# Optimization experiments

Measured on AMD Instinct MI355X. Metric: run time of the kernel, lower is better.

The kernel has to match this reference:

```python
import jax, jax.numpy as jnp
import numpy as np

B = 4096
D = 128
TEMP = 0.5
EPS = 1e-8  # torch cosine_similarity norm clamp


def setup_inputs() -> dict:
    key = jax.random.key(0)
    k1, k2 = jax.random.split(key)
    zi = jax.random.normal(k1, (B, D), dtype=jnp.float32)
    zj = jax.random.normal(k2, (B, D), dtype=jnp.float32)
    return {"zi": zi, "zj": zj}


def reference(zi, zj):
    b = zi.shape[0]
    n2 = 2 * b
    z = jnp.concatenate([zi, zj], axis=0)                      # (2N, D)
    norm = jnp.maximum(jnp.linalg.norm(z, axis=-1, keepdims=True), EPS)
    zn = z / norm
    sim = zn @ zn.T                                            # (2N, 2N) cosine similarity
    # positives: torch.diag(sim, +B) and torch.diag(sim, -B)
    right = jnp.diagonal(sim, offset=b)                        # sim[i, i+B]
    left = jnp.diagonal(sim, offset=-b)                        # sim[i+B, i]
    pos = jnp.concatenate([left, right]) / TEMP                # (2N,)
    # logits row i = [pos_i] + all sims except self-diagonal and the positive,
    # so the softmax denominator set = all entries except the self-diagonal.
    logits = sim / TEMP
    neg_big = jnp.asarray(jnp.finfo(logits.dtype).min, logits.dtype)
    masked = jnp.where(jnp.eye(n2, dtype=bool), neg_big, logits)
    lse = jax.nn.logsumexp(masked, axis=1)                     # (2N,)
    # CrossEntropyLoss(reduction='sum') with label 0, then / 2N
    loss = jnp.sum(lse - pos) / n2
    return loss
```

## Files before the change

### kernel.cpp

```cpp
#include <hip/hip_runtime.h>
#include <hip/hip_bf16.h>


#define BB 4096
#define N2 8192
#define DD 128
#define CSPLIT 16
#define CW (N2 / CSPLIT)
#define NCT (CW / 16)

using bf16 = __hip_bfloat16;
typedef __attribute__((ext_vector_type(8))) short short8;
typedef __attribute__((ext_vector_type(4))) float float4v;

__global__ __launch_bounds__(256) void ntx_norm_kernel(
    const float* __restrict__ zi, const float* __restrict__ zj,
    bf16* __restrict__ zn, float* __restrict__ rowsum, float* __restrict__ pos) {
  const int wave = threadIdx.x >> 6;
  const int lane = threadIdx.x & 63;
  const int row = blockIdx.x * 4 + wave;
  const float* own = (row < BB) ? (zi + (size_t)row * DD)
                                : (zj + (size_t)(row - BB) * DD);
  const float* par = (row < BB) ? (zj + (size_t)row * DD)
                                : (zi + (size_t)(row - BB) * DD);
  float2 v = ((const float2*)own)[lane];
  float2 w = ((const float2*)par)[lane];
  float s1 = v.x * v.x + v.y * v.y;
  float s2 = w.x * w.x + w.y * w.y;
  float s3 = v.x * w.x + v.y * w.y;
  #pragma unroll
  for (int o = 32; o > 0; o >>= 1) {
    s1 += __shfl_xor(s1, o);
    s2 += __shfl_xor(s2, o);
    s3 += __shfl_xor(s3, o);
  }
  float nv = fmaxf(sqrtf(s1), 1e-8f);
  float nw = fmaxf(sqrtf(s2), 1e-8f);
  float rv = 1.0f / nv;
  bf16 bx = __float2bfloat16(v.x * rv);
  bf16 by = __float2bfloat16(v.y * rv);
  __hip_bfloat162 h2; h2.x = bx; h2.y = by;
  ((__hip_bfloat162*)(zn + (size_t)row * DD))[lane] = h2;
  float fx = __bfloat162float(bx), fy = __bfloat162float(by);
  float sii = fx * fx + fy * fy;
  #pragma unroll
  for (int o = 32; o > 0; o >>= 1) sii += __shfl_xor(sii, o);
  if (lane == 0) {
    rowsum[row] = -__expf(2.0f * sii);
    pos[row] = s3 / (nv * nw);
  }
}

__global__ __launch_bounds__(256) void ntx_sim_kernel(
    const bf16* __restrict__ zn, float* __restrict__ rowsum) {
  const int wave = threadIdx.x >> 6;
  const int lane = threadIdx.x & 63;
  const int quad = lane >> 4;
  const int l15  = lane & 15;
  const short* zs = (const short*)zn;

  const int rowBase = blockIdx.y * 256 + wave * 64;
  const int colBase0 = blockIdx.x * CW;

  short8 a[4][4];
  #pragma unroll
  for (int t = 0; t < 4; t++) {
    const short* ap = zs + (size_t)(rowBase + t * 16 + l15) * DD + quad * 8;
    #pragma unroll
    for (int c = 0; c < 4; c++) a[t][c] = *(const short8*)(ap + c * 32);
  }

  float rs[4][4];
  #pragma unroll
  for (int t = 0; t < 4; t++)
    #pragma unroll
    for (int r = 0; r < 4; r++) rs[t][r] = 0.0f;

  const short* bbase = zs + (size_t)(colBase0 + l15) * DD + quad * 8;

  short8 b[4];
  #pragma unroll
  for (int c = 0; c < 4; c++) b[c] = *(const short8*)(bbase + c * 32);

  for (int ct = 0; ct < NCT; ct++) {
    const int nct = (ct + 1) & (NCT - 1);
    const short* bp = bbase + (size_t)nct * 16 * DD;
    short8 bn[4];
    #pragma unroll
    for (int c = 0; c < 4; c++) bn[c] = *(const short8*)(bp + c * 32);

    #pragma unroll
    for (int t = 0; t < 4; t++) {
      float4v acc = {0.f, 0.f, 0.f, 0.f};
      acc = __builtin_amdgcn_mfma_f32_16x16x32_bf16(a[t][0], b[0], acc, 0, 0, 0);
      acc = __builtin_amdgcn_mfma_f32_16x16x32_bf16(a[t][1], b[1], acc, 0, 0, 0);
      acc = __builtin_amdgcn_mfma_f32_16x16x32_bf16(a[t][2], b[2], acc, 0, 0, 0);
      acc = __builtin_amdgcn_mfma_f32_16x16x32_bf16(a[t][3], b[3], acc, 0, 0, 0);
      #pragma unroll
      for (int r = 0; r < 4; r++) rs[t][r] += __expf(acc[r] * 2.0f);
    }

    #pragma unroll
    for (int c = 0; c < 4; c++) b[c] = bn[c];
  }

  #pragma unroll
  for (int t = 0; t < 4; t++) {
    #pragma unroll
    for (int r = 0; r < 4; r++) {
      float s = rs[t][r];
      s += __shfl_xor(s, 1);
      s += __shfl_xor(s, 2);
      s += __shfl_xor(s, 4);
      s += __shfl_xor(s, 8);
      if (l15 == 0)
        atomicAdd(&rowsum[rowBase + t * 16 + quad * 4 + r], s);
    }
  }
}

__global__ __launch_bounds__(1024) void ntx_finalize_kernel(
    const float* __restrict__ rowsum, const float* __restrict__ pos,
    float* __restrict__ out) {
  float s = 0.f;
  for (int i = threadIdx.x; i < N2; i += 1024)
    s += __logf(rowsum[i]) - 2.0f * pos[i];
  #pragma unroll
  for (int o = 32; o > 0; o >>= 1) s += __shfl_xor(s, o);
  __shared__ float sm[16];
  const int wave = threadIdx.x >> 6;
  const int lane = threadIdx.x & 63;
  if (lane == 0) sm[wave] = s;
  __syncthreads();
  if (threadIdx.x == 0) {
    float t = 0.f;
    #pragma unroll
    for (int i = 0; i < 16; i++) t += sm[i];
    out[0] = t / (float)N2;
  }
}

extern "C" void kernel_launch(void* const* d_in, const int* in_sizes, int n_in,
                              void* d_out, int out_size, void* d_ws, size_t ws_size,
                              hipStream_t stream) {
  const float* zi = (const float*)d_in[0];
  const float* zj = (const float*)d_in[1];
  float* out = (float*)d_out;

  char* ws = (char*)d_ws;
  bf16* zn = (bf16*)ws;
  float* rowsum = (float*)(ws + (size_t)N2 * DD * 2);
  float* pos = rowsum + N2;

  ntx_norm_kernel<<<N2 / 4, 256, 0, stream>>>(zi, zj, zn, rowsum, pos);
  dim3 grid(CSPLIT, N2 / 256);
  ntx_sim_kernel<<<grid, 256, 0, stream>>>(zn, rowsum);
  ntx_finalize_kernel<<<1, 1024, 0, stream>>>(rowsum, pos, out);
}
```

Baseline: 100.6 us.

## Stage B tiles in LDS via async DMA, prescale by log2e, fuse finalize

```diff
diff --git a/kernel.cpp b/kernel.cpp
--- a/kernel.cpp
+++ b/kernel.cpp
@@ -1,24 +1,38 @@
 #include <hip/hip_runtime.h>
 #include <hip/hip_bf16.h>
+#include <stdint.h>
 
 
 #define BB 4096
 #define N2 8192
 #define DD 128
-#define CSPLIT 16
+#define CSPLIT 32
 #define CW (N2 / CSPLIT)
-#define NCT (CW / 16)
+#define STAGE 64
+#define NCHUNK (CW / STAGE)
+#define NBLOCKS (CSPLIT * (N2 / 256))
+#define TWO_LOG2E 2.8853900817779268f
 
 using bf16 = __hip_bfloat16;
 typedef __attribute__((ext_vector_type(8))) short short8;
 typedef __attribute__((ext_vector_type(4))) float float4v;
 
+__device__ inline void load_lds16(const void* g, void* l) {
+  __builtin_amdgcn_global_load_lds(
+      (const __attribute__((address_space(1))) uint32_t*)g,
+      (__attribute__((address_space(3))) uint32_t*)(uint32_t)(uintptr_t)l,
+      16, 0, 0);
+}
+
 __global__ __launch_bounds__(256) void ntx_norm_kernel(
     const float* __restrict__ zi, const float* __restrict__ zj,
-    bf16* __restrict__ zn, float* __restrict__ rowsum, float* __restrict__ pos) {
+    bf16* __restrict__ zn, bf16* __restrict__ zn_s,
+    float* __restrict__ rowsum, float* __restrict__ pos,
+    int* __restrict__ counter) {
   const int wave = threadIdx.x >> 6;
   const int lane = threadIdx.x & 63;
   const int row = blockIdx.x * 4 + wave;
+  if (blockIdx.x == 0 && threadIdx.x == 0) counter[0] = 0;
   const float* own = (row < BB) ? (zi + (size_t)row * DD)
                                 : (zj + (size_t)(row - BB) * DD);
   const float* par = (row < BB) ? (zj + (size_t)row * DD)
@@ -39,33 +53,44 @@
   float rv = 1.0f / nv;
   bf16 bx = __float2bfloat16(v.x * rv);
   bf16 by = __float2bfloat16(v.y * rv);
+  bf16 sx = __float2bfloat16(v.x * rv * TWO_LOG2E);
+  bf16 sy = __float2bfloat16(v.y * rv * TWO_LOG2E);
   __hip_bfloat162 h2; h2.x = bx; h2.y = by;
   ((__hip_bfloat162*)(zn + (size_t)row * DD))[lane] = h2;
-  float fx = __bfloat162float(bx), fy = __bfloat162float(by);
-  float sii = fx * fx + fy * fy;
+  __hip_bfloat162 g2; g2.x = sx; g2.y = sy;
+  ((__hip_bfloat162*)(zn_s + (size_t)row * DD))[lane] = g2;
+  float sii = __bfloat162float(sx) * __bfloat162float(bx) +
+              __bfloat162float(sy) * __bfloat162float(by);
   #pragma unroll
   for (int o = 32; o > 0; o >>= 1) sii += __shfl_xor(sii, o);
   if (lane == 0) {
-    rowsum[row] = -__expf(2.0f * sii);
+    rowsum[row] = -__builtin_amdgcn_exp2f(sii);
     pos[row] = s3 / (nv * nw);
   }
 }
 
 __global__ __launch_bounds__(256) void ntx_sim_kernel(
-    const bf16* __restrict__ zn, float* __restrict__ rowsum) {
-  const int wave = threadIdx.x >> 6;
-  const int lane = threadIdx.x & 63;
+    const bf16* __restrict__ zn, const bf16* __restrict__ zn_s,
+    float* __restrict__ rowsum, const float* __restrict__ pos,
+    int* __restrict__ counter, float* __restrict__ out) {
+  __shared__ short lds[2][STAGE * DD];
+  __shared__ int lastFlag;
+  __shared__ float sm[4];
+  const int tid  = threadIdx.x;
+  const int wave = tid >> 6;
+  const int lane = tid & 63;
   const int quad = lane >> 4;
   const int l15  = lane & 15;
-  const short* zs = (const short*)zn;
-
-  const int rowBase = blockIdx.y * 256 + wave * 64;
+  const short* zs  = (const short*)zn;
+  const short* zss = (const short*)zn_s;
+
+  const int rowBase  = blockIdx.y * 256 + wave * 64;
   const int colBase0 = blockIdx.x * CW;
 
   short8 a[4][4];
   #pragma unroll
   for (int t = 0; t < 4; t++) {
-    const short* ap = zs + (size_t)(rowBase + t * 16 + l15) * DD + quad * 8;
+    const short* ap = zss + (size_t)(rowBase + t * 16 + l15) * DD + quad * 8;
     #pragma unroll
     for (int c = 0; c < 4; c++) a[t][c] = *(const short8*)(ap + c * 32);
   }
@@ -76,33 +101,50 @@
     #pragma unroll
     for (int r = 0; r < 4; r++) rs[t][r] = 0.0f;
 
-  const short* bbase = zs + (size_t)(colBase0 + l15) * DD + quad * 8;
-
-  short8 b[4];
-  #pragma unroll
-  for (int c = 0; c < 4; c++) b[c] = *(const short8*)(bbase + c * 32);
-
-  for (int ct = 0; ct < NCT; ct++) {
-    const int nct = (ct + 1) & (NCT - 1);
-    const short* bp = bbase + (size_t)nct * 16 * DD;
-    short8 bn[4];
-    #pragma unroll
-    for (int c = 0; c < 4; c++) bn[c] = *(const short8*)(bp + c * 32);
-
-    #pragma unroll
-    for (int t = 0; t < 4; t++) {
-      float4v acc = {0.f, 0.f, 0.f, 0.f};
-      acc = __builtin_amdgcn_mfma_f32_16x16x32_bf16(a[t][0], b[0], acc, 0, 0, 0);
-      acc = __builtin_amdgcn_mfma_f32_16x16x32_bf16(a[t][1], b[1], acc, 0, 0, 0);
-      acc = __builtin_amdgcn_mfma_f32_16x16x32_bf16(a[t][2], b[2], acc, 0, 0, 0);
-      acc = __builtin_amdgcn_mfma_f32_16x16x32_bf16(a[t][3], b[3], acc, 0, 0, 0);
+  const int swz = (tid & 15) ^ (tid >> 4);
+
+#define DMA(CHUNK, PB)                                                        \
+  do {                                                                        \
+    const char* gbase = (const char*)zs +                                     \
+                        ((size_t)(colBase0 + (CHUNK) * STAGE) << 8);          \
+    char* lbase = (char*)&lds[PB][0];                                         \
+    _Pragma("unroll")                                                         \
+    for (int j = 0; j < 4; j++) {                                             \
+      const int lr = j * 16 + (tid >> 4);                                     \
+      load_lds16(gbase + ((size_t)lr << 8) + (swz << 4),                      \
+                 lbase + j * 4096 + tid * 16);                                \
+    }                                                                         \
+  } while (0)
+
+  DMA(0, 0);
+  __syncthreads();
+
+  for (int c = 0; c < NCHUNK; c++) {
+    if (c + 1 < NCHUNK) DMA(c + 1, (c + 1) & 1);
+    const short* Bb = &lds[c & 1][0];
+    #pragma unroll
+    for (int ct = 0; ct < 4; ct++) {
+      short8 b[4];
       #pragma unroll
-      for (int r = 0; r < 4; r++) rs[t][r] += __expf(acc[r] * 2.0f);
+      for (int kc = 0; kc < 4; kc++) {
+        const int off = (ct * 16 + l15) * DD + (((kc * 4 + quad) ^ l15) << 3);
+        b[kc] = *(const short8*)(Bb + off);
+      }
+      #pragma unroll
+      for (int t = 0; t < 4; t++) {
+        float4v acc = {0.f, 0.f, 0.f, 0.f};
+        acc = __builtin_amdgcn_mfma_f32_16x16x32_bf16(a[t][0], b[0], acc, 0, 0, 0);
+        acc = __builtin_amdgcn_mfma_f32_16x16x32_bf16(a[t][1], b[1], acc, 0, 0, 0);
+        acc = __builtin_amdgcn_mfma_f32_16x16x32_bf16(a[t][2], b[2], acc, 0, 0, 0);
+        acc = __builtin_amdgcn_mfma_f32_16x16x32_bf16(a[t][3], b[3], acc, 0, 0, 0);
+        #pragma unroll
+        for (int r = 0; r < 4; r++)
+          rs[t][r] += __builtin_amdgcn_exp2f(acc[r]);
+      }
     }
-
-    #pragma unroll
-    for (int c = 0; c < 4; c++) b[c] = bn[c];
-  }
+    if (c + 1 < NCHUNK) __syncthreads();
+  }
+#undef DMA
 
   #pragma unroll
   for (int t = 0; t < 4; t++) {
@@ -117,26 +159,28 @@
         atomicAdd(&rowsum[rowBase + t * 16 + quad * 4 + r], s);
     }
   }
-}
-
-__global__ __launch_bounds__(1024) void ntx_finalize_kernel(
-    const float* __restrict__ rowsum, const float* __restrict__ pos,
-    float* __restrict__ out) {
-  float s = 0.f;
-  for (int i = threadIdx.x; i < N2; i += 1024)
-    s += __logf(rowsum[i]) - 2.0f * pos[i];
-  #pragma unroll
-  for (int o = 32; o > 0; o >>= 1) s += __shfl_xor(s, o);
-  __shared__ float sm[16];
-  const int wave = threadIdx.x >> 6;
-  const int lane = threadIdx.x & 63;
-  if (lane == 0) sm[wave] = s;
+
+  __threadfence();
   __syncthreads();
-  if (threadIdx.x == 0) {
-    float t = 0.f;
-    #pragma unroll
-    for (int i = 0; i < 16; i++) t += sm[i];
-    out[0] = t / (float)N2;
+  if (tid == 0) {
+    int old = atomicAdd(counter, 1);
+    lastFlag = (old == NBLOCKS - 1);
+  }
+  __syncthreads();
+  if (lastFlag) {
+    __threadfence();
+    float s = 0.f;
+    for (int i = tid; i < N2; i += 256) {
+      float r = __hip_atomic_load(&rowsum[i], __ATOMIC_RELAXED,
+                                  __HIP_MEMORY_SCOPE_AGENT);
+      s += __logf(r) - 2.0f * pos[i];
+    }
+    #pragma unroll
+    for (int o = 32; o > 0; o >>= 1) s += __shfl_xor(s, o);
+    if (lane == 0) sm[wave] = s;
+    __syncthreads();
+    if (tid == 0)
+      out[0] = (sm[0] + sm[1] + sm[2] + sm[3]) / (float)N2;
   }
 }
 
@@ -148,12 +192,14 @@
   float* out = (float*)d_out;
 
   char* ws = (char*)d_ws;
-  bf16* zn = (bf16*)ws;
-  float* rowsum = (float*)(ws + (size_t)N2 * DD * 2);
+  bf16* zn   = (bf16*)ws;
+  bf16* zn_s = (bf16*)(ws + (size_t)N2 * DD * 2);
+  float* rowsum = (float*)(ws + 2 * (size_t)N2 * DD * 2);
   float* pos = rowsum + N2;
-
-  ntx_norm_kernel<<<N2 / 4, 256, 0, stream>>>(zi, zj, zn, rowsum, pos);
+  int* counter = (int*)(pos + N2);
+
+  ntx_norm_kernel<<<N2 / 4, 256, 0, stream>>>(zi, zj, zn, zn_s, rowsum, pos,
+                                              counter);
   dim3 grid(CSPLIT, N2 / 256);
-  ntx_sim_kernel<<<grid, 256, 0, stream>>>(zn, rowsum);
-  ntx_finalize_kernel<<<1, 1024, 0, stream>>>(rowsum, pos, out);
-}
+  ntx_sim_kernel<<<grid, 256, 0, stream>>>(zn, zn_s, rowsum, pos, counter, out);
+}
```

Result: slower. 159.5 us (+58.5%).
